# Kernel optimization log

Measured on AMD Instinct MI355X. Metric: run time of the kernel, lower is better.

Reference implementation:

```python
import jax, jax.numpy as jnp
import numpy as np


def setup_inputs() -> dict:
    key = jax.random.key(0)
    ks = jax.random.split(key, 7)
    n, d_in, d_h = 1024, 1024, 512
    scale = 1.0 / np.sqrt(d_in)
    return {
        "vectors": jax.random.normal(ks[0], (n, d_in), dtype=jnp.float32),
        "W_h": jax.random.normal(ks[1], (d_h, d_in), dtype=jnp.float32) * scale,
        "b_h": jax.random.normal(ks[2], (d_h,), dtype=jnp.float32) * 0.01,
        "W_m": jax.random.normal(ks[3], (d_h, d_in), dtype=jnp.float32) * scale,
        "b_m": jax.random.normal(ks[4], (d_h,), dtype=jnp.float32) * 0.01,
        "w2": jax.random.normal(ks[5], (d_h,), dtype=jnp.float32) * (1.0 / np.sqrt(d_h)),
        "b2": jax.random.normal(ks[6], (1,), dtype=jnp.float32) * 0.01,
    }


def reference(vectors, W_h, b_h, W_m, b_m, w2, b2):
    # Two linear projections: [n, d_h]
    h = vectors @ W_h.T + b_h  # head representations
    m = vectors @ W_m.T + b_m  # modifier representations
    # Pairwise broadcast add: pair[i, j, :] = h[i] + m[j]  -> [n, n, d_h]
    pair = jnp.tanh(h[:, None, :] + m[None, :, :])
    # Linear to scalar + squeeze -> [n, n]
    scores = jnp.einsum("ijh,h->ij", pair, w2) + b2[0]
    return scores
```

## Files before the change

kernel.cpp:

```cpp
#include <hip/hip_runtime.h>
#include <hip/hip_bf16.h>

#define D_IN  1024
#define D_H   512
#define L2E2  2.885390081777927f
#define ECLAMP 15.0f

typedef _Float16 half8 __attribute__((ext_vector_type(8)));
typedef _Float16 half4v __attribute__((ext_vector_type(4)));
typedef float f32x4 __attribute__((ext_vector_type(4)));

__global__ __launch_bounds__(256) void cvt_kernel(
    const float* __restrict__ V,
    const float* __restrict__ Wh, const float* __restrict__ Wm,
    _Float16* __restrict__ Vh, _Float16* __restrict__ Wf)
{
  const int idx = blockIdx.x * 256 + threadIdx.x;
  {
    float4 x = ((const float4*)V)[idx];
    half4v o = { (_Float16)x.x, (_Float16)x.y, (_Float16)x.z, (_Float16)x.w };
    ((half4v*)Vh)[idx] = o;
  }
  {
    const float4* p = (idx < 131072) ? ((const float4*)Wh + idx)
                                     : ((const float4*)Wm + (idx - 131072));
    float4 x = *p;
    half4v o = { (_Float16)x.x, (_Float16)x.y, (_Float16)x.z, (_Float16)x.w };
    ((half4v*)Wf)[idx] = o;
  }
}

__global__ __launch_bounds__(256, 4) void proj_mfma_kernel(
    const _Float16* __restrict__ Vh, const _Float16* __restrict__ Wf,
    const float* __restrict__ bh, const float* __restrict__ bm,
    float* __restrict__ C)
{
  __shared__ float red[4][32][34];

  const int tid  = threadIdx.x;
  const int lane = tid & 63;
  const int wid  = tid >> 6;
  const int bid  = blockIdx.x;
  const int swz  = (bid & 7) * 128 + (bid >> 3);
  const int i0   = (swz & 31) * 32;
  const int j0   = (swz >> 5) * 32;
  const int r16  = lane & 15;
  const int kg   = lane >> 4;
  const int kb   = wid * 256;

  const _Float16* A0 = Vh + (size_t)(i0 + r16) * 1024 + kb + kg*8;
  const _Float16* A1 = A0 + 16 * 1024;
  const _Float16* B0 = Wf + (size_t)(j0 + r16) * 1024 + kb + kg*8;
  const _Float16* B1 = B0 + 16 * 1024;

  f32x4 acc00 = {0.f,0.f,0.f,0.f}, acc01 = acc00, acc10 = acc00, acc11 = acc00;
  #pragma unroll 4
  for (int k0 = 0; k0 < 256; k0 += 32) {
    half8 a0 = *(const half8*)(A0 + k0);
    half8 a1 = *(const half8*)(A1 + k0);
    half8 b0 = *(const half8*)(B0 + k0);
    half8 b1 = *(const half8*)(B1 + k0);
    acc00 = __builtin_amdgcn_mfma_f32_16x16x32_f16(a0, b0, acc00, 0, 0, 0);
    acc01 = __builtin_amdgcn_mfma_f32_16x16x32_f16(a0, b1, acc01, 0, 0, 0);
    acc10 = __builtin_amdgcn_mfma_f32_16x16x32_f16(a1, b0, acc10, 0, 0, 0);
    acc11 = __builtin_amdgcn_mfma_f32_16x16x32_f16(a1, b1, acc11, 0, 0, 0);
  }

  #pragma unroll
  for (int fi = 0; fi < 2; ++fi) {
    #pragma unroll
    for (int fj = 0; fj < 2; ++fj) {
      const f32x4 acc = (fi == 0) ? (fj == 0 ? acc00 : acc01)
                                  : (fj == 0 ? acc10 : acc11);
      #pragma unroll
      for (int rr = 0; rr < 4; ++rr)
        red[wid][16*fi + 4*kg + rr][16*fj + r16] = acc[rr];
    }
  }
  __syncthreads();

  const int row = tid >> 3;
  const int c4  = (tid & 7) * 4;
  const float* biasp = (j0 < D_H) ? (bh + j0) : (bm + (j0 - D_H));
  float4 bias = *(const float4*)(biasp + c4);
  float4 o;
  #pragma unroll
  for (int q = 0; q < 4; ++q) {
    float s = red[0][row][c4+q] + red[1][row][c4+q]
            + red[2][row][c4+q] + red[3][row][c4+q];
    float x = (s + (&bias.x)[q]) * L2E2;
    x = fminf(fmaxf(x, -ECLAMP), ECLAMP);
    (&o.x)[q] = __builtin_amdgcn_exp2f(x);
  }
  *(float4*)(C + (size_t)(i0 + row) * 1024 + j0 + c4) = o;
}

__global__ __launch_bounds__(256) void proj_kernel(
    const float* __restrict__ V,
    const float* __restrict__ Wh, const float* __restrict__ bh,
    const float* __restrict__ Wm, const float* __restrict__ bm,
    float* __restrict__ C)
{
  __shared__ float As[16][68];
  __shared__ float Bs[16][68];

  const int tid = threadIdx.x;
  const int i0  = (blockIdx.x & 15) * 64, j0 = (blockIdx.x >> 4) * 64;
  const int ti  = tid >> 4, tj = tid & 15;
  const int sr  = tid >> 2;
  const int sk  = (tid & 3) << 2;

  const float* Wbase = (j0 < D_H) ? (Wh + (size_t)j0 * D_IN)
                                  : (Wm + (size_t)(j0 - D_H) * D_IN);
  const float* biasp = (j0 < D_H) ? (bh + j0) : (bm + (j0 - D_H));

  const float* arow = V     + (size_t)(i0 + sr) * D_IN + sk;
  const float* brow = Wbase + (size_t)sr        * D_IN + sk;

  float acc[4][4] = {};
  for (int k0 = 0; k0 < D_IN; k0 += 16) {
    float4 av = *(const float4*)(arow + k0);
    float4 bv = *(const float4*)(brow + k0);
    As[sk+0][sr] = av.x; As[sk+1][sr] = av.y; As[sk+2][sr] = av.z; As[sk+3][sr] = av.w;
    Bs[sk+0][sr] = bv.x; Bs[sk+1][sr] = bv.y; Bs[sk+2][sr] = bv.z; Bs[sk+3][sr] = bv.w;
    __syncthreads();
    #pragma unroll
    for (int kk = 0; kk < 16; ++kk) {
      float4 a = *(const float4*)&As[kk][4*ti];
      float4 b = *(const float4*)&Bs[kk][4*tj];
      #pragma unroll
      for (int x = 0; x < 4; ++x)
        #pragma unroll
        for (int y = 0; y < 4; ++y)
          acc[x][y] = fmaf((&a.x)[x], (&b.x)[y], acc[x][y]);
    }
    __syncthreads();
  }

  const int jl = 4 * tj;
  #pragma unroll
  for (int aa = 0; aa < 4; ++aa) {
    const int i = i0 + 4*ti + aa;
    float4 o;
    #pragma unroll
    for (int bb = 0; bb < 4; ++bb) {
      float x = (acc[aa][bb] + biasp[jl+bb]) * L2E2;
      x = fminf(fmaxf(x, -ECLAMP), ECLAMP);
      (&o.x)[bb] = __builtin_amdgcn_exp2f(x);
    }
    *(float4*)(C + (size_t)i * 1024 + j0 + jl) = o;
  }
}

__global__ __launch_bounds__(256, 2) void score_kernel(
    const float* __restrict__ C,
    const float* __restrict__ w2,
    const float* __restrict__ b2,
    float* __restrict__ out)
{
  __shared__ float hs[2][64][36];
  __shared__ float ms[2][32][36];
  __shared__ float wred[4];

  const int tid = threadIdx.x;
  const int bi  = blockIdx.x & 15;
  const int bj  = blockIdx.x >> 4;
  const int i0  = bi * 64, j0 = bj * 32;
  const int ti  = tid >> 4, tj = tid & 15;

  const int sr  = tid >> 3;
  const int sk  = (tid & 7) << 2;

  float sw = 0.f;
  for (int t = tid; t < D_H; t += 256) sw += w2[t];
  #pragma unroll
  for (int off = 32; off > 0; off >>= 1) sw += __shfl_down(sw, off, 64);
  if ((tid & 63) == 0) wred[tid >> 6] = sw;

  const float* hrow0 = C + (size_t)(i0 + sr)      * 1024 + sk;
  const float* hrow1 = C + (size_t)(i0 + sr + 32) * 1024 + sk;
  const float* mrow  = C + (size_t)(j0 + sr) * 1024 + D_H + sk;

  float4 hv0 = *(const float4*)(hrow0);
  float4 hv1 = *(const float4*)(hrow1);
  float4 mv  = *(const float4*)(mrow);

  float acc[4][2] = {};
  int p = 0;

  float4 ehA[4], emA[2], ehB[4], emB[2];

  #define LOADG(EH, EM, KK)                                            \
  {                                                                    \
    _Pragma("unroll")                                                  \
    for (int a = 0; a < 4; ++a)                                        \
      (EH)[a] = *(const float4*)&hs[p][ti + 16*a][(KK)];               \
    _Pragma("unroll")                                                  \
    for (int c = 0; c < 2; ++c)                                        \
      (EM)[c] = *(const float4*)&ms[p][tj + 16*c][(KK)];               \
  }

  #define COMPG(EH, EM, KB)                                            \
  {                                                                    \
    const float wA = w2[(KB) + 0];                                     \
    const float wB = w2[(KB) + 1];                                     \
    const float wC = w2[(KB) + 2];                                     \
    const float wD = w2[(KB) + 3];                                     \
    _Pragma("unroll")                                                  \
    for (int a = 0; a < 4; ++a) {                                      \
      _Pragma("unroll")                                                \
      for (int c = 0; c < 2; ++c) {                                    \
        float uA = fmaf((EH)[a].x, (EM)[c].x, 1.f);                    \
        float uB = fmaf((EH)[a].y, (EM)[c].y, 1.f);                    \
        float uC = fmaf((EH)[a].z, (EM)[c].z, 1.f);                    \
        float uD = fmaf((EH)[a].w, (EM)[c].w, 1.f);                    \
        float dAB = uA * uB, dCD = uC * uD;                            \
        float nAB = fmaf(wB, uA, wA * uB);                             \
        float nCD = fmaf(wD, uC, wC * uD);                             \
        float den = dAB * dCD;                                         \
        float num = fmaf(nCD, dAB, nAB * dCD);                         \
        acc[a][c] = fmaf(num, __builtin_amdgcn_rcpf(den), acc[a][c]);  \
      }                                                                \
    }                                                                  \
  }

  for (int k0 = 0; k0 < D_H; k0 += 32) {
    *(float4*)&hs[p][sr][sk]      = hv0;
    *(float4*)&hs[p][sr + 32][sk] = hv1;
    *(float4*)&ms[p][sr][sk]      = mv;
    __syncthreads();

    if (k0 + 32 < D_H) {
      hv0 = *(const float4*)(hrow0 + k0 + 32);
      hv1 = *(const float4*)(hrow1 + k0 + 32);
      mv  = *(const float4*)(mrow  + k0 + 32);
    }

    LOADG(ehA, emA, 0)
    #pragma unroll
    for (int gp = 0; gp < 4; ++gp) {
      const int kk = 8 * gp;
      if (gp < 3) { LOADG(ehB, emB, kk + 4) }
      else        { LOADG(ehB, emB, kk + 4) }
      COMPG(ehA, emA, k0 + kk)
      if (gp < 3) { LOADG(ehA, emA, kk + 8) }
      COMPG(ehB, emB, k0 + kk + 4)
    }
    p ^= 1;
  }
  #undef LOADG
  #undef COMPG

  const float base = b2[0] + wred[0] + wred[1] + wred[2] + wred[3];
  #pragma unroll
  for (int a = 0; a < 4; ++a) {
    const int i = i0 + ti + 16*a;
    #pragma unroll
    for (int c = 0; c < 2; ++c) {
      const int j = j0 + tj + 16*c;
      out[(size_t)i * 1024 + j] = fmaf(-2.f, acc[a][c], base);
    }
  }
}

extern "C" void kernel_launch(void* const* d_in, const int* in_sizes, int n_in,
                              void* d_out, int out_size, void* d_ws, size_t ws_size,
                              hipStream_t stream) {
  const float* V  = (const float*)d_in[0];
  const float* Wh = (const float*)d_in[1];
  const float* bh = (const float*)d_in[2];
  const float* Wm = (const float*)d_in[3];
  const float* bm = (const float*)d_in[4];
  const float* w2 = (const float*)d_in[5];
  const float* b2 = (const float*)d_in[6];
  float* outp = (float*)d_out;

  char* ws = (char*)d_ws;
  float* C = (float*)ws;

  if (ws_size >= (size_t)(8u << 20)) {
    _Float16* Vh = (_Float16*)(ws + (4u << 20));
    _Float16* Wf = (_Float16*)(ws + (6u << 20));
    cvt_kernel<<<dim3(1024), dim3(256), 0, stream>>>(V, Wh, Wm, Vh, Wf);
    proj_mfma_kernel<<<dim3(1024), dim3(256), 0, stream>>>(Vh, Wf, bh, bm, C);
  } else {
    proj_kernel<<<dim3(256), dim3(256), 0, stream>>>(V, Wh, bh, Wm, bm, C);
  }
  score_kernel<<<dim3(512), dim3(256), 0, stream>>>(C, w2, b2, outp);
}
```

Measured before the change: 78.25 us.

## Split score reduction over hidden dim into two halves with 64x64 tiles

Adds a score kernel that uses 64x64 output tiles with a 4x4 per-thread register block and splits the 512-wide hidden reduction into two halves. Each half writes a partial score matrix to workspace, and a separate combine kernel sums the two. The larger tile raises reuse of the shared-memory loads, and the split keeps the block count at 512. The cost is an extra 8MB of partial writes and reads, one more kernel launch, and a larger workspace requirement, so this path only runs when at least 16MB of workspace is available.

```diff
diff --git a/kernel.cpp b/kernel.cpp
--- a/kernel.cpp
+++ b/kernel.cpp
@@ -152,7 +152,140 @@
   }
 }
 
-__global__ __launch_bounds__(256, 2) void score_kernel(
+__global__ __launch_bounds__(256) void score_split_kernel(
+    const float* __restrict__ C,
+    const float* __restrict__ w2,
+    const float* __restrict__ b2,
+    float* __restrict__ P0, float* __restrict__ P1)
+{
+  __shared__ float hs[2][64][36];
+  __shared__ float ms[2][64][36];
+  __shared__ float wred[4];
+
+  const int tid  = threadIdx.x;
+  const int b    = blockIdx.x;
+  const int v    = (b & 7) * 64 + (b >> 3);
+  const int tile = v >> 1;
+  const int kh   = v & 1;
+  const int i0   = (tile & 15) * 64;
+  const int j0   = (tile >> 4) * 64;
+  const int kb   = kh * 256;
+  const int ti   = tid >> 4, tj = tid & 15;
+
+  const int sr   = tid >> 3;
+  const int sk   = (tid & 7) << 2;
+
+  if (kh == 0) {
+    float sw = 0.f;
+    for (int t = tid; t < D_H; t += 256) sw += w2[t];
+    #pragma unroll
+    for (int off = 32; off > 0; off >>= 1) sw += __shfl_down(sw, off, 64);
+    if ((tid & 63) == 0) wred[tid >> 6] = sw;
+  }
+
+  const float* hrow0 = C + (size_t)(i0 + sr)      * 1024 + kb + sk;
+  const float* hrow1 = C + (size_t)(i0 + sr + 32) * 1024 + kb + sk;
+  const float* mrow0 = C + (size_t)(j0 + sr)      * 1024 + D_H + kb + sk;
+  const float* mrow1 = C + (size_t)(j0 + sr + 32) * 1024 + D_H + kb + sk;
+
+  float4 hv0 = *(const float4*)(hrow0);
+  float4 hv1 = *(const float4*)(hrow1);
+  float4 mv0 = *(const float4*)(mrow0);
+  float4 mv1 = *(const float4*)(mrow1);
+
+  float acc[4][4] = {};
+  int p = 0;
+
+  float4 ehA[4], emA[4], ehB[4], emB[4];
+
+  #define LOADG(EH, EM, KK)                                            \
+  {                                                                    \
+    _Pragma("unroll")                                                  \
+    for (int a = 0; a < 4; ++a)                                        \
+      (EH)[a] = *(const float4*)&hs[p][ti + 16*a][(KK)];               \
+    _Pragma("unroll")                                                  \
+    for (int c = 0; c < 4; ++c)                                        \
+      (EM)[c] = *(const float4*)&ms[p][tj + 16*c][(KK)];               \
+  }
+
+  #define COMPG(EH, EM, KB)                                            \
+  {                                                                    \
+    const float wA = w2[(KB) + 0];                                     \
+    const float wB = w2[(KB) + 1];                                     \
+    const float wC = w2[(KB) + 2];                                     \
+    const float wD = w2[(KB) + 3];                                     \
+    _Pragma("unroll")                                                  \
+    for (int a = 0; a < 4; ++a) {                                      \
+      _Pragma("unroll")                                                \
+      for (int c = 0; c < 4; ++c) {                                    \
+        float uA = fmaf((EH)[a].x, (EM)[c].x, 1.f);                    \
+        float uB = fmaf((EH)[a].y, (EM)[c].y, 1.f);                    \
+        float uC = fmaf((EH)[a].z, (EM)[c].z, 1.f);                    \
+        float uD = fmaf((EH)[a].w, (EM)[c].w, 1.f);                    \
+        float dAB = uA * uB, dCD = uC * uD;                            \
+        float nAB = fmaf(wB, uA, wA * uB);                             \
+        float nCD = fmaf(wD, uC, wC * uD);                             \
+        float den = dAB * dCD;                                         \
+        float num = fmaf(nCD, dAB, nAB * dCD);                         \
+        acc[a][c] = fmaf(num, __builtin_amdgcn_rcpf(den), acc[a][c]);  \
+      }                                                                \
+    }                                                                  \
+  }
+
+  for (int k0 = 0; k0 < 256; k0 += 32) {
+    *(float4*)&hs[p][sr][sk]      = hv0;
+    *(float4*)&hs[p][sr + 32][sk] = hv1;
+    *(float4*)&ms[p][sr][sk]      = mv0;
+    *(float4*)&ms[p][sr + 32][sk] = mv1;
+    __syncthreads();
+
+    if (k0 + 32 < 256) {
+      hv0 = *(const float4*)(hrow0 + k0 + 32);
+      hv1 = *(const float4*)(hrow1 + k0 + 32);
+      mv0 = *(const float4*)(mrow0 + k0 + 32);
+      mv1 = *(const float4*)(mrow1 + k0 + 32);
+    }
+
+    LOADG(ehA, emA, 0)
+    #pragma unroll
+    for (int gp = 0; gp < 4; ++gp) {
+      const int kk = 8 * gp;
+      LOADG(ehB, emB, kk + 4)
+      COMPG(ehA, emA, kb + k0 + kk)
+      if (gp < 3) { LOADG(ehA, emA, kk + 8) }
+      COMPG(ehB, emB, kb + k0 + kk + 4)
+    }
+    p ^= 1;
+  }
+  #undef LOADG
+  #undef COMPG
+
+  float base = 0.f;
+  if (kh == 0) base = b2[0] + wred[0] + wred[1] + wred[2] + wred[3];
+  float* Pz = kh ? P1 : P0;
+  #pragma unroll
+  for (int a = 0; a < 4; ++a) {
+    const int i = i0 + ti + 16*a;
+    #pragma unroll
+    for (int c = 0; c < 4; ++c) {
+      const int j = j0 + tj + 16*c;
+      Pz[(size_t)i * 1024 + j] = fmaf(-2.f, acc[a][c], base);
+    }
+  }
+}
+
+__global__ __launch_bounds__(256) void combine_kernel(
+    const float* __restrict__ P0, const float* __restrict__ P1,
+    float* __restrict__ out)
+{
+  const int idx = blockIdx.x * 256 + threadIdx.x;
+  float4 a = ((const float4*)P0)[idx];
+  float4 b = ((const float4*)P1)[idx];
+  float4 o = {a.x + b.x, a.y + b.y, a.z + b.z, a.w + b.w};
+  ((float4*)out)[idx] = o;
+}
+
+__global__ __launch_bounds__(256, 2) void score_kernel_r9(
     const float* __restrict__ C,
     const float* __restrict__ w2,
     const float* __restrict__ b2,
@@ -240,8 +373,7 @@
     #pragma unroll
     for (int gp = 0; gp < 4; ++gp) {
       const int kk = 8 * gp;
-      if (gp < 3) { LOADG(ehB, emB, kk + 4) }
-      else        { LOADG(ehB, emB, kk + 4) }
+      LOADG(ehB, emB, kk + 4)
       COMPG(ehA, emA, k0 + kk)
       if (gp < 3) { LOADG(ehA, emA, kk + 8) }
       COMPG(ehB, emB, k0 + kk + 4)
@@ -278,13 +410,23 @@
   char* ws = (char*)d_ws;
   float* C = (float*)ws;
 
-  if (ws_size >= (size_t)(8u << 20)) {
+  if (ws_size >= (size_t)(16u << 20)) {
+    _Float16* Vh = (_Float16*)(ws + (4u << 20));
+    _Float16* Wf = (_Float16*)(ws + (6u << 20));
+    float*    P0 = (float*)(ws + (8u << 20));
+    float*    P1 = (float*)(ws + (12u << 20));
+    cvt_kernel<<<dim3(1024), dim3(256), 0, stream>>>(V, Wh, Wm, Vh, Wf);
+    proj_mfma_kernel<<<dim3(1024), dim3(256), 0, stream>>>(Vh, Wf, bh, bm, C);
+    score_split_kernel<<<dim3(512), dim3(256), 0, stream>>>(C, w2, b2, P0, P1);
+    combine_kernel<<<dim3(1024), dim3(256), 0, stream>>>(P0, P1, outp);
+  } else if (ws_size >= (size_t)(8u << 20)) {
     _Float16* Vh = (_Float16*)(ws + (4u << 20));
     _Float16* Wf = (_Float16*)(ws + (6u << 20));
     cvt_kernel<<<dim3(1024), dim3(256), 0, stream>>>(V, Wh, Wm, Vh, Wf);
     proj_mfma_kernel<<<dim3(1024), dim3(256), 0, stream>>>(Vh, Wf, bh, bm, C);
+    score_kernel_r9<<<dim3(512), dim3(256), 0, stream>>>(C, w2, b2, outp);
   } else {
     proj_kernel<<<dim3(256), dim3(256), 0, stream>>>(V, Wh, bh, Wm, bm, C);
-  }
-  score_kernel<<<dim3(512), dim3(256), 0, stream>>>(C, w2, b2, outp);
-}
+    score_kernel_r9<<<dim3(512), dim3(256), 0, stream>>>(C, w2, b2, outp);
+  }
+}
```

Result: no change. 76.81 us (-1.8%).
